# Optimization experiments

Measured on AMD Instinct MI355X. Metric: run time of the kernel, lower is better.

The kernel has to match this reference:

```python
import jax, jax.numpy as jnp
import numpy as np

N = 100000      # nodes
E = 1600000     # edges (avg degree 16)
F_IN = 64       # num_features
HID = 16        # hidden channels (fixed in module)
OUT = 32        # num_classes
K = 2           # kernel_size (dim=1, degree=1 open B-spline -> 2 basis fns)


def setup_inputs() -> dict:
    key = jax.random.key(0)
    ks = jax.random.split(key, 8)
    return {
        "x": jax.random.normal(ks[0], (N, F_IN), jnp.float32),
        "edge_index": jax.random.randint(ks[1], (2, E), 0, N, dtype=jnp.int64),
        "dropout": 0,  # unused in eval mode (F.dropout training=False)
        "edge_attr": jnp.full((E, 1), 0.1, jnp.float32),  # nt([0.1]) broadcast per edge
        "W1": jax.random.normal(ks[2], (K, F_IN, HID), jnp.float32) / np.sqrt(K * F_IN).astype(np.float32),
        "root1": jax.random.normal(ks[3], (F_IN, HID), jnp.float32) / np.sqrt(F_IN).astype(np.float32),
        "bias1": jnp.zeros((HID,), jnp.float32),
        "W2": jax.random.normal(ks[4], (K, HID, OUT), jnp.float32) / np.sqrt(K * HID).astype(np.float32),
        "root2": jax.random.normal(ks[5], (HID, OUT), jnp.float32) / np.sqrt(HID).astype(np.float32),
        "bias2": jnp.zeros((OUT,), jnp.float32),
    }


def spline_conv(x, edge_index, edge_attr, W, root, bias):
    """SplineConv, dim=1, kernel_size=2, degree=1 open B-spline, aggr='mean'."""
    src, dst = edge_index[0], edge_index[1]
    n = x.shape[0]
    u = edge_attr[:, 0]                                  # [E] pseudo-coords in [0,1]
    # degree-1 open spline, kernel_size=2: frac = u*(ks-1) = u; kernels {0,1}
    basis = jnp.stack([1.0 - u, u], axis=1)              # [E, K]
    # transform at node level (cheaper than gathering raw features per edge)
    h = jnp.einsum('nf,kfo->nko', x, W)                  # [N, K, out]
    msg = jnp.einsum('ek,eko->eo', basis, h[src])        # [E, out]
    summed = jax.ops.segment_sum(msg, dst, num_segments=n)
    deg = jax.ops.segment_sum(jnp.ones_like(u), dst, num_segments=n)
    out = summed / jnp.maximum(deg, 1.0)[:, None]        # mean aggregation
    return out + x @ root + bias                          # root weight + bias


def reference(x, edge_index, dropout, edge_attr, W1, root1, bias1, W2, root2, bias2):
    # dropout is a no-op in eval mode
    h = jax.nn.elu(spline_conv(x, edge_index, edge_attr, W1, root1, bias1))
    h = spline_conv(h, edge_index, edge_attr, W2, root2, bias2)
    return jax.nn.log_softmax(h, axis=1)
```

## Files before the change

### kernel.cpp

```cpp
#include <hip/hip_runtime.h>
#include <math.h>

#define NN 100000
#define NE 1600000
#define F_IN 64
#define HID 16
#define OUTF 32
#define BKT_SHIFT 6
#define BKT_NODES 64
#define NBKT 1563
#define SRCM 0x1FFFF
#define CAP_REG 2048
#define CAP_LDS 1184
#define PBLK2 500
#define EPB2 3200
#define OVF_MAX 4096

__device__ __forceinline__ unsigned bf16r(float f) {
    unsigned u = __float_as_uint(f);
    return (u + 0x7FFFu + ((u >> 16) & 1u)) >> 16;
}
__device__ __forceinline__ float bfa(unsigned p) { return __uint_as_float(p << 16); }
__device__ __forceinline__ float bfd(unsigned p) { return __uint_as_float(p & 0xFFFF0000u); }
__device__ __forceinline__ float bfh(unsigned short v) { return __uint_as_float(((unsigned)v) << 16); }

__device__ __forceinline__ void acc8(uint4 hv, float u, float* s0, float* s1) {
    unsigned w[4] = {hv.x, hv.y, hv.z, hv.w};
#pragma unroll
    for (int q = 0; q < 4; ++q) {
        float lo = __uint_as_float(w[q] << 16);
        float hi = __uint_as_float(w[q] & 0xFFFF0000u);
        s0[2 * q]     += lo; s1[2 * q]     = fmaf(u, lo, s1[2 * q]);
        s0[2 * q + 1] += hi; s1[2 * q + 1] = fmaf(u, hi, s1[2 * q + 1]);
    }
}
__device__ __forceinline__ void acc4(uint4 ap, float u, float* a) {
    unsigned w[4] = {ap.x, ap.y, ap.z, ap.w};
#pragma unroll
    for (int q = 0; q < 4; ++q)
        a[q] += fmaf(u, bfd(w[q]), bfa(w[q]));
}

__global__ __launch_bounds__(256) void zeroG_kernel(int* __restrict__ gcur,
                                                    int* __restrict__ novf) {
    int t = blockIdx.x * 256 + threadIdx.x;
    if (t < NBKT) gcur[t] = 0;
    if (t == NBKT) novf[0] = 0;
}

__global__ __launch_bounds__(1024) void partF_kernel(const int* __restrict__ ei,
                                                     const float* __restrict__ ea,
                                                     int* __restrict__ gcur,
                                                     int* __restrict__ novf,
                                                     int4* __restrict__ ovf,
                                                     int2* __restrict__ bkt) {
    __shared__ int hcnt[NBKT];
    __shared__ int hbase[NBKT];
    __shared__ int lbase[NBKT];
    __shared__ int s[1024];
    __shared__ int2 sbuf[EPB2];
    __shared__ unsigned short bid[EPB2];
    int t = threadIdx.x, blk = blockIdx.x;
    for (int i = t; i < NBKT; i += 1024) hcnt[i] = 0;
    __syncthreads();
    int beg = blk * EPB2;
    int4 d4 = make_int4(0, 0, 0, 0);
    bool act = (4 * t) < EPB2;
    if (act) {
        d4 = *(const int4*)(ei + NE + beg + 4 * t);
        atomicAdd(&hcnt[d4.x >> BKT_SHIFT], 1);
        atomicAdd(&hcnt[d4.y >> BKT_SHIFT], 1);
        atomicAdd(&hcnt[d4.z >> BKT_SHIFT], 1);
        atomicAdd(&hcnt[d4.w >> BKT_SHIFT], 1);
    }
    __syncthreads();
    int i0 = 2 * t, i1 = 2 * t + 1;
    int v0 = (i0 < NBKT) ? hcnt[i0] : 0;
    int v1 = (i1 < NBKT) ? hcnt[i1] : 0;
    s[t] = v0 + v1;
    __syncthreads();
    for (int off = 1; off < 1024; off <<= 1) {
        int xv = (t >= off) ? s[t - off] : 0;
        __syncthreads();
        s[t] += xv;
        __syncthreads();
    }
    int run = (t == 0) ? 0 : s[t - 1];
    if (i0 < NBKT) lbase[i0] = run;
    if (i1 < NBKT) lbase[i1] = run + v0;
    __syncthreads();
    for (int i = t; i < NBKT; i += 1024) {
        int c = hcnt[i];
        hbase[i] = c ? atomicAdd(&gcur[i], c) : 0;
        hcnt[i] = 0;
    }
    __syncthreads();
    if (act) {
        int4 s4 = *(const int4*)(ei + beg + 4 * t);
        float4 u4 = *(const float4*)(ea + beg + 4 * t);
        int dst[4] = {d4.x, d4.y, d4.z, d4.w};
        int src[4] = {s4.x, s4.y, s4.z, s4.w};
        float uu[4] = {u4.x, u4.y, u4.z, u4.w};
#pragma unroll
        for (int k = 0; k < 4; ++k) {
            int b = dst[k] >> BKT_SHIFT;
            int r = atomicAdd(&hcnt[b], 1);
            int lp = lbase[b] + r;
            sbuf[lp] = make_int2(src[k] | ((dst[k] & (BKT_NODES - 1)) << 17),
                                 __float_as_int(uu[k]));
            bid[lp] = (unsigned short)b;
        }
    }
    __syncthreads();
    for (int i = t; i < EPB2; i += 1024) {
        int2 pk = sbuf[i];
        int b = bid[i];
        int p = hbase[b] + (i - lbase[b]);
        if (p < CAP_REG) {
            bkt[(size_t)b * CAP_REG + p] = pk;
        } else {
            int o = atomicAdd(novf, 1);
            if (o < OVF_MAX)
                ovf[o] = make_int4(b * BKT_NODES + (((unsigned)pk.x) >> 17), pk.x & SRCM, pk.y, 0);
        }
    }
}

__global__ __launch_bounds__(256) void proj1_kernel(const float* __restrict__ x,
                                                    const float* __restrict__ W1,
                                                    const float* __restrict__ root1,
                                                    const float* __restrict__ bias1,
                                                    unsigned* __restrict__ ab1p,
                                                    float* __restrict__ r1) {
    __shared__ float w[2 * F_IN * HID];
    __shared__ float wr[F_IN * HID];
    __shared__ float bb[HID];
    for (int i = threadIdx.x; i < 2 * F_IN * HID; i += 256) w[i] = W1[i];
    for (int i = threadIdx.x; i < F_IN * HID; i += 256) wr[i] = root1[i];
    if (threadIdx.x < HID) bb[threadIdx.x] = bias1[threadIdx.x];
    __syncthreads();
    int n = blockIdx.x * 256 + threadIdx.x;
    if (n >= NN) return;
    float accA[HID], accB[HID], accR[HID];
#pragma unroll
    for (int o = 0; o < HID; ++o) { accA[o] = 0.f; accB[o] = 0.f; accR[o] = bb[o]; }
    const float4* xr4 = (const float4*)(x + (size_t)n * F_IN);
    for (int f4 = 0; f4 < F_IN / 4; ++f4) {
        float4 xv4 = xr4[f4];
        float xs[4] = {xv4.x, xv4.y, xv4.z, xv4.w};
#pragma unroll
        for (int q = 0; q < 4; ++q) {
            int f = f4 * 4 + q;
            float xv = xs[q];
            const float* w0 = &w[f * HID];
            const float* w1 = &w[F_IN * HID + f * HID];
            const float* w2 = &wr[f * HID];
#pragma unroll
            for (int o = 0; o < HID; ++o) {
                accA[o] = fmaf(xv, w0[o], accA[o]);
                accB[o] = fmaf(xv, w1[o], accB[o]);
                accR[o] = fmaf(xv, w2[o], accR[o]);
            }
        }
    }
    unsigned* ar = ab1p + (size_t)n * HID;
    float* rr = r1 + (size_t)n * HID;
#pragma unroll
    for (int o = 0; o < HID; ++o) {
        ar[o] = bf16r(accA[o]) | (bf16r(accB[o] - accA[o]) << 16);
        rr[o] = accR[o];
    }
}

__global__ __launch_bounds__(256) void gather1_kernel(const int* __restrict__ gcur,
                                                      const int* __restrict__ novf,
                                                      const int4* __restrict__ ovf,
                                                      int2* __restrict__ bkt,
                                                      const unsigned* __restrict__ ab1p,
                                                      const float* __restrict__ r1,
                                                      unsigned short* __restrict__ h16,
                                                      float* __restrict__ dinv,
                                                      int* __restrict__ segg) {
    __shared__ int2 sorted[CAP_LDS];
    __shared__ int cnt[BKT_NODES], cur[BKT_NODES], segb[BKT_NODES + 1];
    __shared__ float degsL[BKT_NODES];
    int t = threadIdx.x;
    int b = blockIdx.x;
    int tot = gcur[b];
    int beg = b * CAP_REG;
    if (t < BKT_NODES) { cnt[t] = 0; cur[t] = 0; degsL[t] = 0.f; }
    __syncthreads();
    int nodeBase = b * BKT_NODES;

    if (tot <= CAP_LDS) {
        for (int e = t; e < tot; e += 256)
            atomicAdd(&cnt[((unsigned)bkt[beg + e].x) >> 17], 1);
        __syncthreads();
        if (t < BKT_NODES) {
            int v = cnt[t];
            int sc = v;
#pragma unroll
            for (int off = 1; off < 64; off <<= 1) {
                int o = __shfl_up(sc, off, 64);
                if (t >= off) sc += o;
            }
            segb[t] = sc - v;
            if (t == 63) segb[64] = sc;
        }
        __syncthreads();
        for (int e = t; e < tot; e += 256) {
            int2 pk = bkt[beg + e];
            int loc = ((unsigned)pk.x) >> 17;
            int pos = segb[loc] + atomicAdd(&cur[loc], 1);
            sorted[pos] = pk;
        }
        __syncthreads();
        int nv = tot >> 1;
        int4* s4 = (int4*)sorted;
        int4* o4 = (int4*)(bkt + beg);
        for (int i = t; i < nv; i += 256) o4[i] = s4[i];
        if (t == 0 && (tot & 1)) bkt[beg + tot - 1] = sorted[tot - 1];
        if (t <= BKT_NODES) segg[b * (BKT_NODES + 1) + t] = segb[t];
        int node = t >> 2;
        int jq = t & 3;
        int s0 = segb[node], e2 = segb[node + 1];
        float acc[4] = {0.f, 0.f, 0.f, 0.f};
        int e = s0;
        for (; e + 3 < e2; e += 4) {
            int2 p0 = sorted[e];
            int2 p1 = sorted[e + 1];
            int2 p2 = sorted[e + 2];
            int2 p3 = sorted[e + 3];
            uint4 a0 = *(const uint4*)(ab1p + ((size_t)(p0.x & SRCM) << 4) + (jq << 2));
            uint4 a1 = *(const uint4*)(ab1p + ((size_t)(p1.x & SRCM) << 4) + (jq << 2));
            uint4 a2 = *(const uint4*)(ab1p + ((size_t)(p2.x & SRCM) << 4) + (jq << 2));
            uint4 a3 = *(const uint4*)(ab1p + ((size_t)(p3.x & SRCM) << 4) + (jq << 2));
            acc4(a0, __int_as_float(p0.y), acc);
            acc4(a1, __int_as_float(p1.y), acc);
            acc4(a2, __int_as_float(p2.y), acc);
            acc4(a3, __int_as_float(p3.y), acc);
        }
        for (; e < e2; ++e) {
            int2 pk = sorted[e];
            uint4 ap = *(const uint4*)(ab1p + ((size_t)(pk.x & SRCM) << 4) + (jq << 2));
            acc4(ap, __int_as_float(pk.y), acc);
        }
        int n = nodeBase + node;
        if (n < NN) {
            float d0 = 1.f / (float)max(e2 - s0, 1);
            float4 rv = *(const float4*)(r1 + ((size_t)n << 4) + (jq << 2));
            float rr[4] = {rv.x, rv.y, rv.z, rv.w};
            unsigned hw[4];
#pragma unroll
            for (int k = 0; k < 4; ++k) {
                float v = acc[k] * d0 + rr[k];
                hw[k] = bf16r(v > 0.f ? v : expm1f(v));
            }
            *(uint2*)(h16 + ((size_t)n << 4) + (jq << 2)) =
                make_uint2(hw[0] | (hw[1] << 16), hw[2] | (hw[3] << 16));
            if (jq == 0) dinv[n] = d0;
        }
    } else {
        float* accL = (float*)sorted;
        int inreg = min(tot, CAP_REG);
        int end = beg + inreg;
        for (int i = t; i < BKT_NODES * HID; i += 256) accL[i] = 0.f;
        __syncthreads();
        int j = t & (HID - 1);
        int g = t >> 4;
        for (int e = beg + g; e < end; e += 16) {
            int2 pk = bkt[e];
            unsigned p = ab1p[(size_t)(pk.x & SRCM) * HID + j];
            atomicAdd(&accL[(((unsigned)pk.x) >> 17) * HID + j],
                      fmaf(__int_as_float(pk.y), bfd(p), bfa(p)));
            if (j == 0) atomicAdd(&degsL[((unsigned)pk.x) >> 17], 1.f);
        }
        int ovn = min(novf[0], OVF_MAX);
        for (int o = 0; o < ovn; ++o) {
            int4 ent = ovf[o];
            int loc = ent.x - nodeBase;
            if (loc >= 0 && loc < BKT_NODES && g == 0) {
                unsigned p = ab1p[(size_t)ent.y * HID + j];
                atomicAdd(&accL[loc * HID + j], fmaf(__int_as_float(ent.z), bfd(p), bfa(p)));
                if (j == 0) atomicAdd(&degsL[loc], 1.f);
            }
        }
        __syncthreads();
        if (t < BKT_NODES) degsL[t] = 1.f / fmaxf(degsL[t], 1.f);
        if (t == 0) segg[b * (BKT_NODES + 1)] = -1;
        __syncthreads();
        for (int idx = t; idx < BKT_NODES * HID; idx += 256) {
            int nl = idx >> 4, jj = idx & (HID - 1);
            int n = nodeBase + nl;
            if (n < NN) {
                float v = accL[idx] * degsL[nl] + r1[(size_t)n * HID + jj];
                h16[(size_t)n * HID + jj] = (unsigned short)bf16r(v > 0.f ? v : expm1f(v));
            }
        }
        if (t < BKT_NODES && nodeBase + t < NN) dinv[nodeBase + t] = degsL[t];
    }
}

#define HB_NODES 32
__global__ __launch_bounds__(256) void gather2_kernel(const int* __restrict__ gcur,
                                                      const int* __restrict__ novf,
                                                      const int4* __restrict__ ovf,
                                                      const int2* __restrict__ bkt,
                                                      const unsigned short* __restrict__ h16,
                                                      const float* __restrict__ W2,
                                                      const float* __restrict__ root2,
                                                      const float* __restrict__ bias2,
                                                      const float* __restrict__ dinv,
                                                      const int* __restrict__ segg,
                                                      float* __restrict__ out) {
    __shared__ float w20[HID * OUTF], w2d[HID * OUTF], wr[HID * OUTF];
    __shared__ float bb[OUTF];
    __shared__ int segb[HB_NODES + 1];
    __shared__ int sflag;
    int t = threadIdx.x;
    int b2 = blockIdx.x;
    int b = b2 >> 1;
    int h = b2 & 1;
    for (int i = t; i < HID * OUTF; i += 256) {
        float a = W2[i];
        w20[i] = a;
        w2d[i] = W2[HID * OUTF + i] - a;
        wr[i] = root2[i];
    }
    if (t < OUTF) bb[t] = bias2[t];
    int tot = gcur[b];
    int beg = b * CAP_REG;
    int nodeBase = b * BKT_NODES + h * HB_NODES;
    if (t <= HB_NODES) segb[t] = segg[b * (BKT_NODES + 1) + h * HB_NODES + t];
    if (t == 0) sflag = segg[b * (BKT_NODES + 1)];
    __syncthreads();

    int node = t >> 3;
    int li = t & 7;
    int sub = li >> 1;
    int jh = li & 1;
    float S0[8] = {0.f, 0.f, 0.f, 0.f, 0.f, 0.f, 0.f, 0.f};
    float S1[8] = {0.f, 0.f, 0.f, 0.f, 0.f, 0.f, 0.f, 0.f};

    if (tot <= CAP_LDS && sflag != -1) {
        const int2* sp = bkt + beg;
        int s = segb[node], e2 = segb[node + 1];
        int e = s + sub;
        for (; e + 12 < e2; e += 16) {
            int2 p0 = sp[e];
            int2 p1 = sp[e + 4];
            int2 p2 = sp[e + 8];
            int2 p3 = sp[e + 12];
            uint4 h0 = *(const uint4*)(h16 + ((size_t)(p0.x & SRCM) << 4) + (jh << 3));
            uint4 h1 = *(const uint4*)(h16 + ((size_t)(p1.x & SRCM) << 4) + (jh << 3));
            uint4 h2 = *(const uint4*)(h16 + ((size_t)(p2.x & SRCM) << 4) + (jh << 3));
            uint4 h3 = *(const uint4*)(h16 + ((size_t)(p3.x & SRCM) << 4) + (jh << 3));
            acc8(h0, __int_as_float(p0.y), S0, S1);
            acc8(h1, __int_as_float(p1.y), S0, S1);
            acc8(h2, __int_as_float(p2.y), S0, S1);
            acc8(h3, __int_as_float(p3.y), S0, S1);
        }
        for (; e < e2; e += 4) {
            int2 pk = sp[e];
            uint4 hv = *(const uint4*)(h16 + ((size_t)(pk.x & SRCM) << 4) + (jh << 3));
            acc8(hv, __int_as_float(pk.y), S0, S1);
        }
#pragma unroll
        for (int k = 0; k < 8; ++k) {
            S0[k] += __shfl_xor(S0[k], 2); S0[k] += __shfl_xor(S0[k], 4);
            S1[k] += __shfl_xor(S1[k], 2); S1[k] += __shfl_xor(S1[k], 4);
        }
    } else {
        float* s0L = w20;
        float* s1L = w2d;
        for (int i = t; i < HB_NODES * HID; i += 256) { s0L[i] = 0.f; s1L[i] = 0.f; }
        __syncthreads();
        int j = t & (HID - 1);
        int g = t >> 4;
        int inreg = min(tot, CAP_REG);
        int end = beg + inreg;
        for (int e = beg + g; e < end; e += 16) {
            int2 pk = bkt[e];
            int loc = ((unsigned)pk.x) >> 17;
            if ((loc >> 5) == h) {
                float hvv = bfh(h16[(size_t)(pk.x & SRCM) * HID + j]);
                atomicAdd(&s0L[(loc & 31) * HID + j], hvv);
                atomicAdd(&s1L[(loc & 31) * HID + j], __int_as_float(pk.y) * hvv);
            }
        }
        int ovn = min(novf[0], OVF_MAX);
        for (int o = 0; o < ovn; ++o) {
            int4 ent = ovf[o];
            int loc = ent.x - nodeBase;
            if (loc >= 0 && loc < HB_NODES && g == 0) {
                float hvv = bfh(h16[(size_t)ent.y * HID + j]);
                atomicAdd(&s0L[loc * HID + j], hvv);
                atomicAdd(&s1L[loc * HID + j], __int_as_float(ent.z) * hvv);
            }
        }
        __syncthreads();
#pragma unroll
        for (int k = 0; k < 8; ++k) {
            S0[k] = s0L[node * HID + jh * 8 + k];
            S1[k] = s1L[node * HID + jh * 8 + k];
        }
        __syncthreads();
        for (int i = t; i < HID * OUTF; i += 256) {
            float a = W2[i];
            w20[i] = a;
            w2d[i] = W2[HID * OUTF + i] - a;
        }
        __syncthreads();
    }

    float F0[16], F1[16];
#pragma unroll
    for (int k = 0; k < 8; ++k) {
        float p0 = __shfl_xor(S0[k], 1);
        float p1 = __shfl_xor(S1[k], 1);
        F0[k] = jh ? p0 : S0[k];
        F0[8 + k] = jh ? S0[k] : p0;
        F1[k] = jh ? p1 : S1[k];
        F1[8 + k] = jh ? S1[k] : p1;
    }
    int n = nodeBase + node;
    if (n < NN) {
        float di = dinv[n];
        uint4 hA = *(const uint4*)(h16 + ((size_t)n << 4));
        uint4 hB = *(const uint4*)(h16 + ((size_t)n << 4) + 8);
        float hf[16];
        unsigned wa[4] = {hA.x, hA.y, hA.z, hA.w};
        unsigned wb[4] = {hB.x, hB.y, hB.z, hB.w};
#pragma unroll
        for (int q = 0; q < 4; ++q) {
            hf[2 * q]     = __uint_as_float(wa[q] << 16);
            hf[2 * q + 1] = __uint_as_float(wa[q] & 0xFFFF0000u);
            hf[8 + 2 * q]     = __uint_as_float(wb[q] << 16);
            hf[8 + 2 * q + 1] = __uint_as_float(wb[q] & 0xFFFF0000u);
        }
        float outv[4];
#pragma unroll
        for (int q = 0; q < 4; ++q) {
            int jj = li * 4 + q;
            float ms = 0.f;
#pragma unroll
            for (int f = 0; f < HID; ++f)
                ms += F0[f] * w20[f * OUTF + jj] + F1[f] * w2d[f * OUTF + jj];
            float v = ms * di + bb[jj];
#pragma unroll
            for (int f = 0; f < HID; ++f)
                v = fmaf(hf[f], wr[f * OUTF + jj], v);
            outv[q] = v;
        }
        float m = fmaxf(fmaxf(outv[0], outv[1]), fmaxf(outv[2], outv[3]));
        m = fmaxf(m, __shfl_xor(m, 1));
        m = fmaxf(m, __shfl_xor(m, 2));
        m = fmaxf(m, __shfl_xor(m, 4));
        float sl = expf(outv[0] - m) + expf(outv[1] - m) + expf(outv[2] - m) + expf(outv[3] - m);
        sl += __shfl_xor(sl, 1);
        sl += __shfl_xor(sl, 2);
        sl += __shfl_xor(sl, 4);
        float lse = m + logf(sl);
        *(float4*)(out + (size_t)n * OUTF + li * 4) =
            make_float4(outv[0] - lse, outv[1] - lse, outv[2] - lse, outv[3] - lse);
    }
}

extern "C" void kernel_launch(void* const* d_in, const int* in_sizes, int n_in,
                              void* d_out, int out_size, void* d_ws, size_t ws_size,
                              hipStream_t stream) {
    const float* x     = (const float*)d_in[0];
    const int*   ei    = (const int*)d_in[1];
    const float* ea    = (const float*)d_in[3];
    const float* W1    = (const float*)d_in[4];
    const float* root1 = (const float*)d_in[5];
    const float* bias1 = (const float*)d_in[6];
    const float* W2    = (const float*)d_in[7];
    const float* root2 = (const float*)d_in[8];
    const float* bias2 = (const float*)d_in[9];
    float* out = (float*)d_out;
    float* ws  = (float*)d_ws;

    const size_t N = NN;
    int*            gcur = (int*)(ws);
    int*            novf = (int*)(ws + 2000);
    int4*           ovf  = (int4*)(ws + 2048);
    float*          dinv = ws + 20000;
    int*            segg = (int*)(ws + 120000);
    float*          r1   = ws + 222000;
    unsigned*       ab1p = (unsigned*)(ws + 222000 + 16 * N);
    unsigned short* h16  = (unsigned short*)(ws + 222000 + 32 * N);
    int2*           bkt  = (int2*)(ws + 222000 + 40 * N);

    int nbN = (NN + 255) / 256;
    zeroG_kernel<<<(NBKT + 256) / 256, 256, 0, stream>>>(gcur, novf);
    partF_kernel<<<PBLK2, 1024, 0, stream>>>(ei, ea, gcur, novf, ovf, bkt);
    proj1_kernel<<<nbN, 256, 0, stream>>>(x, W1, root1, bias1, ab1p, r1);
    gather1_kernel<<<NBKT, 256, 0, stream>>>(gcur, novf, ovf, bkt, ab1p, r1, h16, dinv, segg);
    gather2_kernel<<<NBKT * 2, 256, 0, stream>>>(gcur, novf, ovf, bkt, h16, W2, root2, bias2, dinv, segg, out);
}
```

Baseline: 117.3 us.

## Fold zeroing into projection, halve partition chunk, use wave-shuffle scan in partition

```diff
diff --git a/kernel.cpp b/kernel.cpp
--- a/kernel.cpp
+++ b/kernel.cpp
@@ -12,8 +12,8 @@
 #define SRCM 0x1FFFF
 #define CAP_REG 2048
 #define CAP_LDS 1184
-#define PBLK2 500
-#define EPB2 3200
+#define PBLK2 1000
+#define EPB2 1600
 #define OVF_MAX 4096
 
 __device__ __forceinline__ unsigned bf16r(float f) {
@@ -39,13 +39,6 @@
 #pragma unroll
     for (int q = 0; q < 4; ++q)
         a[q] += fmaf(u, bfd(w[q]), bfa(w[q]));
-}
-
-__global__ __launch_bounds__(256) void zeroG_kernel(int* __restrict__ gcur,
-                                                    int* __restrict__ novf) {
-    int t = blockIdx.x * 256 + threadIdx.x;
-    if (t < NBKT) gcur[t] = 0;
-    if (t == NBKT) novf[0] = 0;
 }
 
 __global__ __launch_bounds__(1024) void partF_kernel(const int* __restrict__ ei,
@@ -55,13 +48,12 @@
                                                      int4* __restrict__ ovf,
                                                      int2* __restrict__ bkt) {
     __shared__ int hcnt[NBKT];
-    __shared__ int hbase[NBKT];
-    __shared__ int lbase[NBKT];
-    __shared__ int s[1024];
+    __shared__ int cur[NBKT];
+    __shared__ int lbase[NBKT + 1];
+    __shared__ int pw[16];
     __shared__ int2 sbuf[EPB2];
-    __shared__ unsigned short bid[EPB2];
     int t = threadIdx.x, blk = blockIdx.x;
-    for (int i = t; i < NBKT; i += 1024) hcnt[i] = 0;
+    for (int i = t; i < NBKT; i += 1024) { hcnt[i] = 0; cur[i] = 0; }
     __syncthreads();
     int beg = blk * EPB2;
     int4 d4 = make_int4(0, 0, 0, 0);
@@ -77,22 +69,37 @@
     int i0 = 2 * t, i1 = 2 * t + 1;
     int v0 = (i0 < NBKT) ? hcnt[i0] : 0;
     int v1 = (i1 < NBKT) ? hcnt[i1] : 0;
-    s[t] = v0 + v1;
-    __syncthreads();
-    for (int off = 1; off < 1024; off <<= 1) {
-        int xv = (t >= off) ? s[t - off] : 0;
-        __syncthreads();
-        s[t] += xv;
-        __syncthreads();
-    }
-    int run = (t == 0) ? 0 : s[t - 1];
-    if (i0 < NBKT) lbase[i0] = run;
-    if (i1 < NBKT) lbase[i1] = run + v0;
-    __syncthreads();
-    for (int i = t; i < NBKT; i += 1024) {
+    int ts = v0 + v1;
+    int lane = t & 63, wid = t >> 6;
+    int sc = ts;
+#pragma unroll
+    for (int off = 1; off < 64; off <<= 1) {
+        int o = __shfl_up(sc, off, 64);
+        if (lane >= off) sc += o;
+    }
+    if (lane == 63) pw[wid] = sc;
+    __syncthreads();
+    if (t < 16) {
+        int p = pw[t];
+        int q = p;
+#pragma unroll
+        for (int off = 1; off < 16; off <<= 1) {
+            int o = __shfl_up(q, off, 64);
+            if (t >= off) q += o;
+        }
+        pw[t] = q - p;
+    }
+    __syncthreads();
+    int ebase = pw[wid] + (sc - ts);
+    if (i0 < NBKT) lbase[i0] = ebase;
+    if (i1 < NBKT) lbase[i1] = ebase + v0;
+    if (t == 0) lbase[NBKT] = EPB2;
+    __syncthreads();
+    int rot = (blk * 397) % NBKT;
+    for (int k = t; k < NBKT; k += 1024) {
+        int i = k + rot; if (i >= NBKT) i -= NBKT;
         int c = hcnt[i];
-        hbase[i] = c ? atomicAdd(&gcur[i], c) : 0;
-        hcnt[i] = 0;
+        hcnt[i] = c ? (atomicAdd(&gcur[i], c) - lbase[i]) : 0;
     }
     __syncthreads();
     if (act) {
@@ -104,18 +111,21 @@
 #pragma unroll
         for (int k = 0; k < 4; ++k) {
             int b = dst[k] >> BKT_SHIFT;
-            int r = atomicAdd(&hcnt[b], 1);
-            int lp = lbase[b] + r;
-            sbuf[lp] = make_int2(src[k] | ((dst[k] & (BKT_NODES - 1)) << 17),
-                                 __float_as_int(uu[k]));
-            bid[lp] = (unsigned short)b;
+            int r = atomicAdd(&cur[b], 1);
+            sbuf[lbase[b] + r] = make_int2(src[k] | ((dst[k] & (BKT_NODES - 1)) << 17),
+                                           __float_as_int(uu[k]));
         }
     }
     __syncthreads();
     for (int i = t; i < EPB2; i += 1024) {
+        int lo = 0, hi = NBKT - 1;
+        while (lo < hi) {
+            int mid = (lo + hi + 1) >> 1;
+            if (lbase[mid] <= i) lo = mid; else hi = mid - 1;
+        }
+        int b = lo;
         int2 pk = sbuf[i];
-        int b = bid[i];
-        int p = hbase[b] + (i - lbase[b]);
+        int p = hcnt[b] + i;
         if (p < CAP_REG) {
             bkt[(size_t)b * CAP_REG + p] = pk;
         } else {
@@ -126,12 +136,17 @@
     }
 }
 
-__global__ __launch_bounds__(256) void proj1_kernel(const float* __restrict__ x,
-                                                    const float* __restrict__ W1,
-                                                    const float* __restrict__ root1,
-                                                    const float* __restrict__ bias1,
-                                                    unsigned* __restrict__ ab1p,
-                                                    float* __restrict__ r1) {
+__global__ __launch_bounds__(256) void proj1z_kernel(const float* __restrict__ x,
+                                                     const float* __restrict__ W1,
+                                                     const float* __restrict__ root1,
+                                                     const float* __restrict__ bias1,
+                                                     unsigned* __restrict__ ab1p,
+                                                     float* __restrict__ r1,
+                                                     int* __restrict__ gcur,
+                                                     int* __restrict__ novf) {
+    int gz = blockIdx.x * 256 + threadIdx.x;
+    if (gz < NBKT) gcur[gz] = 0;
+    if (gz == NBKT) novf[0] = 0;
     __shared__ float w[2 * F_IN * HID];
     __shared__ float wr[F_IN * HID];
     __shared__ float bb[HID];
@@ -493,9 +508,8 @@
     int2*           bkt  = (int2*)(ws + 222000 + 40 * N);
 
     int nbN = (NN + 255) / 256;
-    zeroG_kernel<<<(NBKT + 256) / 256, 256, 0, stream>>>(gcur, novf);
+    proj1z_kernel<<<nbN, 256, 0, stream>>>(x, W1, root1, bias1, ab1p, r1, gcur, novf);
     partF_kernel<<<PBLK2, 1024, 0, stream>>>(ei, ea, gcur, novf, ovf, bkt);
-    proj1_kernel<<<nbN, 256, 0, stream>>>(x, W1, root1, bias1, ab1p, r1);
     gather1_kernel<<<NBKT, 256, 0, stream>>>(gcur, novf, ovf, bkt, ab1p, r1, h16, dinv, segg);
     gather2_kernel<<<NBKT * 2, 256, 0, stream>>>(gcur, novf, ovf, bkt, h16, W2, root2, bias2, dinv, segg, out);
 }
```

After: 119.1 us. No clear change (+1.6%).
